# Kernel tuning notes

Hardware: AMD Instinct MI355X
Metric: run time of the kernel (lower is better)

## Reference

```python
import jax, jax.numpy as jnp
import numpy as np

D_MODEL = 1024
N_HEADS = 16
D_HEAD = D_MODEL // N_HEADS
B, T = 2, 2048


def setup_inputs() -> dict:
    key = jax.random.key(0)
    ks = jax.random.split(key, 8)
    s = 1.0 / np.sqrt(D_MODEL)
    return {
        "x": jax.random.normal(ks[0], (B, T, D_MODEL), dtype=jnp.float32),
        "ln_g": jnp.ones((D_MODEL,), jnp.float32),
        "ln_b": jnp.zeros((D_MODEL,), jnp.float32),
        "w_qkv": jax.random.normal(ks[1], (D_MODEL, 3 * D_MODEL), jnp.float32) * s,
        "b_qkv": jnp.zeros((3 * D_MODEL,), jnp.float32),
        "w_gate": jax.random.normal(ks[2], (D_MODEL, D_MODEL), jnp.float32) * s,
        "b_gate": jnp.zeros((D_MODEL,), jnp.float32),
        "w_proj": jax.random.normal(ks[3], (D_MODEL, D_MODEL), jnp.float32) * s,
        "b_proj": jnp.zeros((D_MODEL,), jnp.float32),
    }


def reference(x, ln_g, ln_b, w_qkv, b_qkv, w_gate, b_gate, w_proj, b_proj):
    Bb, Tt, Dd = x.shape
    H, dh = N_HEADS, D_HEAD

    # LayerNorm (eps=1e-5, torch default)
    mu = jnp.mean(x, axis=-1, keepdims=True)
    var = jnp.mean((x - mu) ** 2, axis=-1, keepdims=True)
    x_norm = (x - mu) / jnp.sqrt(var + 1e-5) * ln_g + ln_b

    qkv = x_norm @ w_qkv + b_qkv
    q, k, v = jnp.split(qkv, 3, axis=-1)

    # concept gate on the RAW input x (not x_norm), normalized by its mean
    gate_sig = jax.nn.sigmoid(x @ w_gate + b_gate)
    gate_norm = gate_sig / (jnp.mean(gate_sig, axis=-1, keepdims=True) + 1e-5)
    q = q * gate_norm
    k = k * gate_norm

    # [B,T,D] -> [B,H,T,dh]
    def to_heads(t):
        return t.reshape(Bb, Tt, H, dh).transpose(0, 2, 1, 3)

    q, k, v = to_heads(q), to_heads(k), to_heads(v)

    q = jax.nn.elu(q) + 1.0
    k = jax.nn.elu(k) + 1.0

    # materialized outer-product cumsum (faithful to source formulation)
    kv = jnp.einsum("bhtd,bhtm->bhtdm", k, v)          # [B,H,T,dh,dh]
    kv_cumsum = jnp.cumsum(kv, axis=2)
    out_num = jnp.einsum("bhtd,bhtdm->bhtm", q, kv_cumsum)
    k_cumsum = jnp.cumsum(k, axis=2)
    out_den = jnp.einsum("bhtd,bhtd->bht", q, k_cumsum)[..., None] + 1e-5
    out = out_num / out_den                              # [B,H,T,dh]

    out = out.transpose(0, 2, 1, 3).reshape(Bb, Tt, Dd)
    return out @ w_proj + b_proj
```

## Files before the change

kernel.cpp:

```cpp
#include <hip/hip_runtime.h>
#include <math.h>

constexpr int D      = 1024;
constexpr int H      = 16;
constexpr int DH     = 64;
constexpr int Bb     = 2;
constexpr int T      = 2048;
constexpr int BT     = Bb * T;
constexpr int CHUNK  = 64;
constexpr int NC     = T / CHUNK;
constexpr int LS     = 72;

typedef __attribute__((ext_vector_type(8))) short bf16x8;
typedef __attribute__((ext_vector_type(4))) float f32x4;

#define GLOAD_LDS16(gp, lp) \
    __builtin_amdgcn_global_load_lds((const __attribute__((address_space(1))) void*)(gp), \
                                     (__attribute__((address_space(3))) void*)(lp), 16, 0, 0)

__device__ __forceinline__ short to_bf16(float f) {
    unsigned u = __float_as_uint(f);
    unsigned r = (u + 0x7fffu + ((u >> 16) & 1u)) >> 16;
    return (short)r;
}
__device__ __forceinline__ float bf2f(short s) {
    return __uint_as_float(((unsigned)(unsigned short)s) << 16);
}

__device__ __forceinline__ float block_sum_256(float v, float* sbuf) {
    #pragma unroll
    for (int off = 32; off > 0; off >>= 1) v += __shfl_down(v, off, 64);
    int lane = threadIdx.x & 63;
    int wid  = threadIdx.x >> 6;
    if (lane == 0) sbuf[wid] = v;
    __syncthreads();
    float r = (threadIdx.x < 4) ? sbuf[threadIdx.x] : 0.0f;
    r += __shfl_down(r, 2, 64);
    r += __shfl_down(r, 1, 64);
    if (threadIdx.x == 0) sbuf[0] = r;
    __syncthreads();
    float outv = sbuf[0];
    __syncthreads();
    return outv;
}

__device__ __forceinline__ float elu1(float x) {
    return x > 0.0f ? x + 1.0f : expf(x);
}

__global__ __launch_bounds__(256) void ln_kernel(const float* __restrict__ x,
                                                 const float* __restrict__ g,
                                                 const float* __restrict__ b,
                                                 short* __restrict__ ynb,
                                                 short* __restrict__ xb) {
    __shared__ float sbuf[4];
    int row = blockIdx.x;
    const float* xr = x + (size_t)row * D;
    int c = threadIdx.x * 4;
    float4 xv = *(const float4*)(xr + c);
    float mu = block_sum_256(xv.x + xv.y + xv.z + xv.w, sbuf) * (1.0f / D);
    float d0 = xv.x - mu, d1 = xv.y - mu, d2 = xv.z - mu, d3 = xv.w - mu;
    float var = block_sum_256(d0*d0 + d1*d1 + d2*d2 + d3*d3, sbuf) * (1.0f / D);
    float rstd = rsqrtf(var + 1e-5f);
    float4 gv = *(const float4*)(g + c);
    float4 bv = *(const float4*)(b + c);
    short4 o, xo;
    o.x = to_bf16(d0 * rstd * gv.x + bv.x);
    o.y = to_bf16(d1 * rstd * gv.y + bv.y);
    o.z = to_bf16(d2 * rstd * gv.z + bv.z);
    o.w = to_bf16(d3 * rstd * gv.w + bv.w);
    xo.x = to_bf16(xv.x); xo.y = to_bf16(xv.y);
    xo.z = to_bf16(xv.z); xo.w = to_bf16(xv.w);
    *(short4*)(ynb + (size_t)row * D + c) = o;
    *(short4*)(xb  + (size_t)row * D + c) = xo;
}

__global__ __launch_bounds__(256) void transpose_all_kernel(const float* __restrict__ wq,
                                                            const float* __restrict__ wg,
                                                            const float* __restrict__ wp,
                                                            short* __restrict__ wTcomb,
                                                            short* __restrict__ wTp) {
    __shared__ short tile[32][33];
    int bid = blockIdx.x;
    const float* W; short* Wt; int N; int t;
    if (bid < 3072)      { W = wq; Wt = wTcomb;                        N = 3072; t = bid; }
    else if (bid < 4096) { W = wg; Wt = wTcomb + (size_t)3072 * 1024;  N = 1024; t = bid - 3072; }
    else                 { W = wp; Wt = wTp;                           N = 1024; t = bid - 4096; }
    int ntiles = N >> 5;
    int nb = (t % ntiles) * 32, kb = (t / ntiles) * 32;
    int tx = threadIdx.x & 31, ty = threadIdx.x >> 5;
    #pragma unroll
    for (int i = 0; i < 4; ++i) {
        int k = kb + ty + i * 8;
        tile[ty + i * 8][tx] = to_bf16(W[(size_t)k * N + nb + tx]);
    }
    __syncthreads();
    #pragma unroll
    for (int i = 0; i < 4; ++i) {
        int n = nb + ty + i * 8;
        Wt[(size_t)n * 1024 + kb + tx] = tile[tx][ty + i * 8];
    }
}

__global__ __launch_bounds__(256) void gemm_fused_qkvgate(const short* __restrict__ xnb,
                                                          const short* __restrict__ xb,
                                                          const short* __restrict__ Wt,
                                                          const float* __restrict__ b_qkv,
                                                          const float* __restrict__ b_gate,
                                                          short* __restrict__ qkvb,
                                                          short* __restrict__ gateb) {
    constexpr int BK = 32, K = 1024;
    __shared__ short Als[128 * BK];
    __shared__ short Bls[128 * BK];

    const int tid  = threadIdx.x;
    const int wave = tid >> 6;
    const int lane = tid & 63;
    const int row0 = blockIdx.y * 128;
    const int col0 = blockIdx.x * 128;
    const bool isg = (col0 >= 3 * D);
    const short* A = isg ? xb : xnb;
    const int wm = (wave & 1) * 64;
    const int wn = (wave >> 1) * 64;

    f32x4 acc[4][4] = {};
    const int srow = lane >> 2;
    const int skk  = (lane & 3) * 8;
    const int fr = lane & 15;
    const int fk = (lane >> 4) * 8;

    for (int k0 = 0; k0 < K; k0 += BK) {
        __syncthreads();
        #pragma unroll
        for (int u = 0; u < 2; ++u) {
            int cchunk = wave * 2 + u;
            int r = cchunk * 16 + srow;
            GLOAD_LDS16(A  + (size_t)(row0 + r) * K + k0 + skk, &Als[cchunk * 512]);
            GLOAD_LDS16(Wt + (size_t)(col0 + r) * K + k0 + skk, &Bls[cchunk * 512]);
        }
        __syncthreads();

        bf16x8 af[4], bfr[4];
        #pragma unroll
        for (int i = 0; i < 4; ++i) {
            af[i]  = *(const bf16x8*)&Als[(wm + i * 16 + fr) * BK + fk];
            bfr[i] = *(const bf16x8*)&Bls[(wn + i * 16 + fr) * BK + fk];
        }
        #pragma unroll
        for (int mi = 0; mi < 4; ++mi)
            #pragma unroll
            for (int ni = 0; ni < 4; ++ni)
                acc[mi][ni] = __builtin_amdgcn_mfma_f32_16x16x32_bf16(af[mi], bfr[ni], acc[mi][ni], 0, 0, 0);
    }

    const int ccol  = lane & 15;
    const int crow4 = (lane >> 4) * 4;
    const float* biasp = isg ? (b_gate - 3 * D) : b_qkv;
    short* dst  = isg ? gateb : qkvb;
    const int stride = isg ? D : 3 * D;
    const int csub   = isg ? 3 * D : 0;
    #pragma unroll
    for (int mi = 0; mi < 4; ++mi) {
        #pragma unroll
        for (int ni = 0; ni < 4; ++ni) {
            int col = col0 + wn + ni * 16 + ccol;
            float bv = biasp[col];
            #pragma unroll
            for (int r = 0; r < 4; ++r) {
                int row = row0 + wm + mi * 16 + crow4 + r;
                dst[(size_t)row * stride + (col - csub)] = to_bf16(acc[mi][ni][r] + bv);
            }
        }
    }
}

__global__ __launch_bounds__(256) void gate_apply_inplace(short* __restrict__ qkvb,
                                                          const short* __restrict__ gateb) {
    __shared__ float sbuf[4];
    int row = blockIdx.x;
    int c = threadIdx.x * 4;
    short4 gl = *(const short4*)(gateb + (size_t)row * D + c);
    float s0 = 1.0f / (1.0f + expf(-bf2f(gl.x)));
    float s1 = 1.0f / (1.0f + expf(-bf2f(gl.y)));
    float s2 = 1.0f / (1.0f + expf(-bf2f(gl.z)));
    float s3 = 1.0f / (1.0f + expf(-bf2f(gl.w)));
    float mean = block_sum_256(s0 + s1 + s2 + s3, sbuf) * (1.0f / D);
    float inv = 1.0f / (mean + 1e-5f);
    float g0 = s0 * inv, g1 = s1 * inv, g2 = s2 * inv, g3 = s3 * inv;

    short* qp = qkvb + (size_t)row * (3 * D) + c;
    short* kp = qp + D;
    short4 qv = *(short4*)qp;
    short4 kv = *(short4*)kp;
    qv.x = to_bf16(elu1(bf2f(qv.x) * g0)); qv.y = to_bf16(elu1(bf2f(qv.y) * g1));
    qv.z = to_bf16(elu1(bf2f(qv.z) * g2)); qv.w = to_bf16(elu1(bf2f(qv.w) * g3));
    kv.x = to_bf16(elu1(bf2f(kv.x) * g0)); kv.y = to_bf16(elu1(bf2f(kv.y) * g1));
    kv.z = to_bf16(elu1(bf2f(kv.z) * g2)); kv.w = to_bf16(elu1(bf2f(kv.w) * g3));
    *(short4*)qp = qv;
    *(short4*)kp = kv;
}

__global__ __launch_bounds__(256) void chunk_state_mfma(const short* __restrict__ qkvb,
                                                        float* __restrict__ SxT,
                                                        float* __restrict__ zbuf) {
    __shared__ short Kt[DH * LS];
    __shared__ short Vt[DH * LS];
    int idx = blockIdx.x;
    int c = idx & (NC - 1), h = (idx >> 5) & (H - 1), b = idx >> 9;
    size_t bt0 = (size_t)b * T + c * CHUNK;
    const short* kbase = qkvb + bt0 * (3 * D) + D + h * DH;
    const short* vbase = qkvb + bt0 * (3 * D) + 2 * D + h * DH;
    int tid = threadIdx.x;

    #pragma unroll
    for (int l = 0; l < 2; ++l) {
        int i  = tid + l * 256;
        int t  = i >> 3;
        int d8 = (i & 7) * 8;
        bf16x8 kv = *(const bf16x8*)(kbase + (size_t)t * (3 * D) + d8);
        bf16x8 vv = *(const bf16x8*)(vbase + (size_t)t * (3 * D) + d8);
        #pragma unroll
        for (int j = 0; j < 8; ++j) {
            Kt[(d8 + j) * LS + t] = kv[j];
            Vt[(d8 + j) * LS + t] = vv[j];
        }
    }
    __syncthreads();

    const int wv = tid >> 6, lane = tid & 63;
    const int fr = lane & 15, quad = lane >> 4;
    const int fk = quad * 8, crow4 = quad * 4, ccol = lane & 15;
    const int mbase = wv * 16;

    bf16x8 af[2];
    af[0] = *(const bf16x8*)&Vt[(mbase + fr) * LS + fk];
    af[1] = *(const bf16x8*)&Vt[(mbase + fr) * LS + 32 + fk];

    f32x4 acc[4] = {};
    #pragma unroll
    for (int n = 0; n < 4; ++n) {
        #pragma unroll
        for (int ck = 0; ck < 2; ++ck) {
            bf16x8 bk = *(const bf16x8*)&Kt[(n * 16 + fr) * LS + ck * 32 + fk];
            acc[n] = __builtin_amdgcn_mfma_f32_16x16x32_bf16(af[ck], bk, acc[n], 0, 0, 0);
        }
    }

    float* Sd = SxT + (size_t)idx * (DH * DH);
    #pragma unroll
    for (int n = 0; n < 4; ++n)
        #pragma unroll
        for (int r = 0; r < 4; ++r)
            Sd[(mbase + crow4 + r) * DH + n * 16 + ccol] = acc[n][r];

    if (tid < DH) {
        float zs = 0.0f;
        for (int t = 0; t < CHUNK; ++t) zs += bf2f(Kt[tid * LS + t]);
        zbuf[(size_t)idx * DH + tid] = zs;
    }
}

__global__ __launch_bounds__(256) void chunk_prefix_kernel(const float* __restrict__ S,
                                                           short* __restrict__ Spb,
                                                           float* __restrict__ z) {
    int bh   = blockIdx.x >> 4;
    int part = blockIdx.x & 15;
    int e    = part * 256 + threadIdx.x;
    const float* Sb = S + (size_t)bh * NC * DH * DH;
    short* Pb = Spb + (size_t)bh * NC * DH * DH;
    float acc = 0.0f;
    for (int c = 0; c < NC; ++c) {
        size_t off = (size_t)c * DH * DH + e;
        float t = Sb[off];
        Pb[off] = to_bf16(acc);
        acc += t;
    }
    if (part == 0 && threadIdx.x < DH) {
        float* zb = z + (size_t)bh * NC * DH;
        float za = 0.0f;
        for (int c = 0; c < NC; ++c) {
            float* p = zb + c * DH + threadIdx.x;
            float t = *p; *p = za; za += t;
        }
    }
}

__global__ __launch_bounds__(256) void chunk_attn_mfma(const short* __restrict__ qkvb,
                                                       const short* __restrict__ Spb,
                                                       const float* __restrict__ zbuf,
                                                       short* __restrict__ attnb) {
    __shared__ short Qs[CHUNK * LS];
    __shared__ short Ks[CHUNK * LS];
    __shared__ short Vt[DH * LS];
    __shared__ short Ss[DH * LS];
    __shared__ short As[CHUNK * LS];
    __shared__ float zpL[DH];
    __shared__ float den[CHUNK];

    int idx = blockIdx.x;
    int c = idx & (NC - 1), h = (idx >> 5) & (H - 1), b = idx >> 9;
    size_t bt0 = (size_t)b * T + c * CHUNK;
    const short* qbase = qkvb + bt0 * (3 * D) + h * DH;
    const short* kbase = qbase + D;
    const short* vbase = qbase + 2 * D;
    const short* spb = Spb + (size_t)idx * (DH * DH);
    int tid = threadIdx.x;

    #pragma unroll
    for (int l = 0; l < 2; ++l) {
        int i  = tid + l * 256;
        int t  = i >> 3;
        int d8 = (i & 7) * 8;
        *(bf16x8*)&Qs[t * LS + d8] = *(const bf16x8*)(qbase + (size_t)t * (3 * D) + d8);
        *(bf16x8*)&Ks[t * LS + d8] = *(const bf16x8*)(kbase + (size_t)t * (3 * D) + d8);
        bf16x8 vv = *(const bf16x8*)(vbase + (size_t)t * (3 * D) + d8);
        #pragma unroll
        for (int j = 0; j < 8; ++j) Vt[(d8 + j) * LS + t] = vv[j];
        *(bf16x8*)&Ss[t * LS + d8] = *(const bf16x8*)(spb + (size_t)i * 8);
    }
    if (tid < DH) zpL[tid] = zbuf[(size_t)idx * DH + tid];
    __syncthreads();

    const int wv = tid >> 6, lane = tid & 63;
    const int fr = lane & 15, quad = lane >> 4;
    const int fk = quad * 8, crow4 = quad * 4, ccol = lane & 15;
    const int tbase = wv * 16;

    bf16x8 aq[2];
    aq[0] = *(const bf16x8*)&Qs[(tbase + fr) * LS + fk];
    aq[1] = *(const bf16x8*)&Qs[(tbase + fr) * LS + 32 + fk];

    f32x4 accs[4] = {};
    #pragma unroll
    for (int n = 0; n < 4; ++n) {
        #pragma unroll
        for (int ck = 0; ck < 2; ++ck) {
            bf16x8 bk = *(const bf16x8*)&Ks[(n * 16 + fr) * LS + ck * 32 + fk];
            accs[n] = __builtin_amdgcn_mfma_f32_16x16x32_bf16(aq[ck], bk, accs[n], 0, 0, 0);
        }
    }

    float part[4] = {0.f, 0.f, 0.f, 0.f};
    #pragma unroll
    for (int n = 0; n < 4; ++n) {
        #pragma unroll
        for (int r = 0; r < 4; ++r) {
            int tt = tbase + crow4 + r;
            int ss = n * 16 + ccol;
            float v = (ss <= tt) ? accs[n][r] : 0.0f;
            part[r] += v;
            As[tt * LS + ss] = to_bf16(v);
        }
    }
    #pragma unroll
    for (int r = 0; r < 4; ++r) {
        part[r] += __shfl_xor(part[r], 1, 64);
        part[r] += __shfl_xor(part[r], 2, 64);
        part[r] += __shfl_xor(part[r], 4, 64);
        part[r] += __shfl_xor(part[r], 8, 64);
    }
    if (fr == 0) {
        #pragma unroll
        for (int r = 0; r < 4; ++r) den[tbase + crow4 + r] = part[r];
    }
    __syncthreads();

    if (tid < CHUNK) {
        float qz = 0.0f;
        #pragma unroll 8
        for (int d = 0; d < DH; ++d) qz += bf2f(Qs[tid * LS + d]) * zpL[d];
        den[tid] += qz + 1e-5f;
    }

    f32x4 acco[4] = {};
    #pragma unroll
    for (int m4 = 0; m4 < 4; ++m4) {
        #pragma unroll
        for (int ck = 0; ck < 2; ++ck) {
            bf16x8 bs = *(const bf16x8*)&Ss[(m4 * 16 + fr) * LS + ck * 32 + fk];
            acco[m4] = __builtin_amdgcn_mfma_f32_16x16x32_bf16(aq[ck], bs, acco[m4], 0, 0, 0);
        }
    }
    bf16x8 aa[2];
    aa[0] = *(const bf16x8*)&As[(tbase + fr) * LS + fk];
    aa[1] = *(const bf16x8*)&As[(tbase + fr) * LS + 32 + fk];
    #pragma unroll
    for (int m4 = 0; m4 < 4; ++m4) {
        #pragma unroll
        for (int ck = 0; ck < 2; ++ck) {
            bf16x8 bv = *(const bf16x8*)&Vt[(m4 * 16 + fr) * LS + ck * 32 + fk];
            acco[m4] = __builtin_amdgcn_mfma_f32_16x16x32_bf16(aa[ck], bv, acco[m4], 0, 0, 0);
        }
    }
    __syncthreads();

    short* obase = attnb + bt0 * D + h * DH;
    #pragma unroll
    for (int r = 0; r < 4; ++r) {
        int tt = tbase + crow4 + r;
        float rv = 1.0f / den[tt];
        #pragma unroll
        for (int m4 = 0; m4 < 4; ++m4)
            obase[(size_t)tt * D + m4 * 16 + ccol] = to_bf16(acco[m4][r] * rv);
    }
}

__global__ __launch_bounds__(256) void gemm_proj64(const short* __restrict__ A,
                                                   const short* __restrict__ Bt,
                                                   const float* __restrict__ bias,
                                                   float* __restrict__ C) {
    constexpr int BK = 32, K = 1024, N = 1024;
    __shared__ short Als[64 * BK];
    __shared__ short Bls[128 * BK];

    const int tid  = threadIdx.x;
    const int wave = tid >> 6;
    const int lane = tid & 63;
    const int row0 = blockIdx.y * 64;
    const int col0 = blockIdx.x * 128;
    const int wn = wave * 32;

    f32x4 acc[4][2] = {};
    const int srow = lane >> 2;
    const int skk  = (lane & 3) * 8;
    const int fr = lane & 15;
    const int fk = (lane >> 4) * 8;

    for (int k0 = 0; k0 < K; k0 += BK) {
        __syncthreads();
        #pragma unroll
        for (int u = 0; u < 3; ++u) {
            int cc = wave * 3 + u;
            if (cc < 4) {
                int r = cc * 16 + srow;
                GLOAD_LDS16(A + (size_t)(row0 + r) * K + k0 + skk, &Als[cc * 512]);
            } else {
                int c2 = cc - 4;
                int r = c2 * 16 + srow;
                GLOAD_LDS16(Bt + (size_t)(col0 + r) * K + k0 + skk, &Bls[c2 * 512]);
            }
        }
        __syncthreads();

        bf16x8 af[4], bfr[2];
        #pragma unroll
        for (int i = 0; i < 4; ++i) af[i] = *(const bf16x8*)&Als[(i * 16 + fr) * BK + fk];
        #pragma unroll
        for (int j = 0; j < 2; ++j) bfr[j] = *(const bf16x8*)&Bls[(wn + j * 16 + fr) * BK + fk];
        #pragma unroll
        for (int mi = 0; mi < 4; ++mi)
            #pragma unroll
            for (int ni = 0; ni < 2; ++ni)
                acc[mi][ni] = __builtin_amdgcn_mfma_f32_16x16x32_bf16(af[mi], bfr[ni], acc[mi][ni], 0, 0, 0);
    }

    const int ccol  = lane & 15;
    const int crow4 = (lane >> 4) * 4;
    #pragma unroll
    for (int mi = 0; mi < 4; ++mi) {
        #pragma unroll
        for (int ni = 0; ni < 2; ++ni) {
            int col = col0 + wn + ni * 16 + ccol;
            float bv = bias[col];
            #pragma unroll
            for (int r = 0; r < 4; ++r) {
                int row = row0 + mi * 16 + crow4 + r;
                C[(size_t)row * N + col] = acc[mi][ni][r] + bv;
            }
        }
    }
}

extern "C" void kernel_launch(void* const* d_in, const int* in_sizes, int n_in,
                              void* d_out, int out_size, void* d_ws, size_t ws_size,
                              hipStream_t stream) {
    const float* x      = (const float*)d_in[0];
    const float* ln_g   = (const float*)d_in[1];
    const float* ln_b   = (const float*)d_in[2];
    const float* w_qkv  = (const float*)d_in[3];
    const float* b_qkv  = (const float*)d_in[4];
    const float* w_gate = (const float*)d_in[5];
    const float* b_gate = (const float*)d_in[6];
    const float* w_proj = (const float*)d_in[7];
    const float* b_proj = (const float*)d_in[8];
    float* out = (float*)d_out;

    short* xnb   = (short*)d_ws;
    short* xb    = xnb + (size_t)BT * D;
    short* wTc   = xb + (size_t)BT * D;
    short* wTp   = wTc + (size_t)4096 * 1024;
    short* qkvb  = wTp + (size_t)D * D;
    short* gateb = qkvb + (size_t)BT * 3 * D;
    short* attnb = gateb + (size_t)BT * D;
    float* zbuf  = (float*)(attnb + (size_t)BT * D);
    float* SxT   = (float*)xnb;
    short* Spb   = wTc;

    ln_kernel<<<BT, 256, 0, stream>>>(x, ln_g, ln_b, xnb, xb);
    transpose_all_kernel<<<5120, 256, 0, stream>>>(w_qkv, w_gate, w_proj, wTc, wTp);
    gemm_fused_qkvgate<<<dim3(32, 32), 256, 0, stream>>>(
        xnb, xb, wTc, b_qkv, b_gate, qkvb, gateb);
    gate_apply_inplace<<<BT, 256, 0, stream>>>(qkvb, gateb);
    chunk_state_mfma<<<Bb * H * NC, 256, 0, stream>>>(qkvb, SxT, zbuf);
    chunk_prefix_kernel<<<Bb * H * 16, 256, 0, stream>>>(SxT, Spb, zbuf);
    chunk_attn_mfma<<<Bb * H * NC, 256, 0, stream>>>(qkvb, Spb, zbuf, attnb);
    gemm_proj64<<<dim3(D / 128, BT / 64), 256, 0, stream>>>(attnb, wTp, b_proj, out);
}
```

Before: 209.9 us.

## Merge LN and transpose kernels, deepen GEMM K tiles, fold chunk prefix into attention

Merges the layernorm and weight-transpose kernels into one launch, and doubles the K tile of both GEMMs to 64 so each loop iteration issues twice as many MFMAs per barrier pair. It also removes the separate chunk-prefix kernel: each attention block now sums the preceding chunk states and z vectors from fp32 global memory itself. This saves two launches and a serial prefix pass. In exchange, later chunks read up to 31 prior states each, which is redundant global traffic that grows with chunk index.

```diff
diff --git a/kernel.cpp b/kernel.cpp
--- a/kernel.cpp
+++ b/kernel.cpp
@@ -48,57 +48,59 @@
     return x > 0.0f ? x + 1.0f : expf(x);
 }
 
-__global__ __launch_bounds__(256) void ln_kernel(const float* __restrict__ x,
-                                                 const float* __restrict__ g,
-                                                 const float* __restrict__ b,
-                                                 short* __restrict__ ynb,
-                                                 short* __restrict__ xb) {
+__global__ __launch_bounds__(256) void pre_kernel(const float* __restrict__ x,
+                                                  const float* __restrict__ g,
+                                                  const float* __restrict__ b,
+                                                  const float* __restrict__ wq,
+                                                  const float* __restrict__ wg,
+                                                  const float* __restrict__ wp,
+                                                  short* __restrict__ ynb,
+                                                  short* __restrict__ xbb,
+                                                  short* __restrict__ wTcomb,
+                                                  short* __restrict__ wTp) {
     __shared__ float sbuf[4];
-    int row = blockIdx.x;
-    const float* xr = x + (size_t)row * D;
-    int c = threadIdx.x * 4;
-    float4 xv = *(const float4*)(xr + c);
-    float mu = block_sum_256(xv.x + xv.y + xv.z + xv.w, sbuf) * (1.0f / D);
-    float d0 = xv.x - mu, d1 = xv.y - mu, d2 = xv.z - mu, d3 = xv.w - mu;
-    float var = block_sum_256(d0*d0 + d1*d1 + d2*d2 + d3*d3, sbuf) * (1.0f / D);
-    float rstd = rsqrtf(var + 1e-5f);
-    float4 gv = *(const float4*)(g + c);
-    float4 bv = *(const float4*)(b + c);
-    short4 o, xo;
-    o.x = to_bf16(d0 * rstd * gv.x + bv.x);
-    o.y = to_bf16(d1 * rstd * gv.y + bv.y);
-    o.z = to_bf16(d2 * rstd * gv.z + bv.z);
-    o.w = to_bf16(d3 * rstd * gv.w + bv.w);
-    xo.x = to_bf16(xv.x); xo.y = to_bf16(xv.y);
-    xo.z = to_bf16(xv.z); xo.w = to_bf16(xv.w);
-    *(short4*)(ynb + (size_t)row * D + c) = o;
-    *(short4*)(xb  + (size_t)row * D + c) = xo;
-}
-
-__global__ __launch_bounds__(256) void transpose_all_kernel(const float* __restrict__ wq,
-                                                            const float* __restrict__ wg,
-                                                            const float* __restrict__ wp,
-                                                            short* __restrict__ wTcomb,
-                                                            short* __restrict__ wTp) {
     __shared__ short tile[32][33];
     int bid = blockIdx.x;
-    const float* W; short* Wt; int N; int t;
-    if (bid < 3072)      { W = wq; Wt = wTcomb;                        N = 3072; t = bid; }
-    else if (bid < 4096) { W = wg; Wt = wTcomb + (size_t)3072 * 1024;  N = 1024; t = bid - 3072; }
-    else                 { W = wp; Wt = wTp;                           N = 1024; t = bid - 4096; }
-    int ntiles = N >> 5;
-    int nb = (t % ntiles) * 32, kb = (t / ntiles) * 32;
-    int tx = threadIdx.x & 31, ty = threadIdx.x >> 5;
-    #pragma unroll
-    for (int i = 0; i < 4; ++i) {
-        int k = kb + ty + i * 8;
-        tile[ty + i * 8][tx] = to_bf16(W[(size_t)k * N + nb + tx]);
-    }
-    __syncthreads();
-    #pragma unroll
-    for (int i = 0; i < 4; ++i) {
-        int n = nb + ty + i * 8;
-        Wt[(size_t)n * 1024 + kb + tx] = tile[tx][ty + i * 8];
+    if (bid < BT) {
+        int row = bid;
+        const float* xr = x + (size_t)row * D;
+        int c = threadIdx.x * 4;
+        float4 xv = *(const float4*)(xr + c);
+        float mu = block_sum_256(xv.x + xv.y + xv.z + xv.w, sbuf) * (1.0f / D);
+        float d0 = xv.x - mu, d1 = xv.y - mu, d2 = xv.z - mu, d3 = xv.w - mu;
+        float var = block_sum_256(d0*d0 + d1*d1 + d2*d2 + d3*d3, sbuf) * (1.0f / D);
+        float rstd = rsqrtf(var + 1e-5f);
+        float4 gv = *(const float4*)(g + c);
+        float4 bv = *(const float4*)(b + c);
+        short4 o, xo;
+        o.x = to_bf16(d0 * rstd * gv.x + bv.x);
+        o.y = to_bf16(d1 * rstd * gv.y + bv.y);
+        o.z = to_bf16(d2 * rstd * gv.z + bv.z);
+        o.w = to_bf16(d3 * rstd * gv.w + bv.w);
+        xo.x = to_bf16(xv.x); xo.y = to_bf16(xv.y);
+        xo.z = to_bf16(xv.z); xo.w = to_bf16(xv.w);
+        *(short4*)(ynb + (size_t)row * D + c) = o;
+        *(short4*)(xbb + (size_t)row * D + c) = xo;
+    } else {
+        int t2 = bid - BT;
+        const float* W; short* Wt; int N; int t;
+        if (t2 < 3072)      { W = wq; Wt = wTcomb;                       N = 3072; t = t2; }
+        else if (t2 < 4096) { W = wg; Wt = wTcomb + (size_t)3072 * 1024; N = 1024; t = t2 - 3072; }
+        else                { W = wp; Wt = wTp;                          N = 1024; t = t2 - 4096; }
+        int ntiles = N >> 5;
+        int nb = (t % ntiles) * 32, kb = (t / ntiles) * 32;
+        int tx = threadIdx.x & 31, ty = threadIdx.x >> 5;
+        #pragma unroll
+        for (int i = 0; i < 4; ++i) {
+            int k = kb + ty + i * 8;
+            tile[ty + i * 8][tx] = to_bf16(W[(size_t)k * N + nb + tx]);
+        }
+        __syncthreads();
+        #pragma unroll
+        for (int i = 0; i < 4; ++i) {
+            int n = nb + ty + i * 8;
+            Wt[(size_t)n * 1024 + kb + tx] = tile[tx][ty + i * 8];
+        }
     }
 }
 
@@ -109,7 +111,7 @@
                                                           const float* __restrict__ b_gate,
                                                           short* __restrict__ qkvb,
                                                           short* __restrict__ gateb) {
-    constexpr int BK = 32, K = 1024;
+    constexpr int BK = 64, K = 1024;
     __shared__ short Als[128 * BK];
     __shared__ short Bls[128 * BK];
 
@@ -124,33 +126,36 @@
     const int wn = (wave >> 1) * 64;
 
     f32x4 acc[4][4] = {};
-    const int srow = lane >> 2;
-    const int skk  = (lane & 3) * 8;
+    const int srow = lane >> 3;
+    const int skk  = (lane & 7) * 8;
     const int fr = lane & 15;
     const int fk = (lane >> 4) * 8;
 
     for (int k0 = 0; k0 < K; k0 += BK) {
         __syncthreads();
         #pragma unroll
-        for (int u = 0; u < 2; ++u) {
-            int cchunk = wave * 2 + u;
-            int r = cchunk * 16 + srow;
+        for (int u = 0; u < 4; ++u) {
+            int cchunk = wave * 4 + u;
+            int r = cchunk * 8 + srow;
             GLOAD_LDS16(A  + (size_t)(row0 + r) * K + k0 + skk, &Als[cchunk * 512]);
             GLOAD_LDS16(Wt + (size_t)(col0 + r) * K + k0 + skk, &Bls[cchunk * 512]);
         }
         __syncthreads();
 
-        bf16x8 af[4], bfr[4];
-        #pragma unroll
-        for (int i = 0; i < 4; ++i) {
-            af[i]  = *(const bf16x8*)&Als[(wm + i * 16 + fr) * BK + fk];
-            bfr[i] = *(const bf16x8*)&Bls[(wn + i * 16 + fr) * BK + fk];
-        }
-        #pragma unroll
-        for (int mi = 0; mi < 4; ++mi)
-            #pragma unroll
-            for (int ni = 0; ni < 4; ++ni)
-                acc[mi][ni] = __builtin_amdgcn_mfma_f32_16x16x32_bf16(af[mi], bfr[ni], acc[mi][ni], 0, 0, 0);
+        #pragma unroll
+        for (int h = 0; h < 2; ++h) {
+            bf16x8 af[4], bfr[4];
+            #pragma unroll
+            for (int i = 0; i < 4; ++i) {
+                af[i]  = *(const bf16x8*)&Als[(wm + i * 16 + fr) * BK + h * 32 + fk];
+                bfr[i] = *(const bf16x8*)&Bls[(wn + i * 16 + fr) * BK + h * 32 + fk];
+            }
+            #pragma unroll
+            for (int mi = 0; mi < 4; ++mi)
+                #pragma unroll
+                for (int ni = 0; ni < 4; ++ni)
+                    acc[mi][ni] = __builtin_amdgcn_mfma_f32_16x16x32_bf16(af[mi], bfr[ni], acc[mi][ni], 0, 0, 0);
+        }
     }
 
     const int ccol  = lane & 15;
@@ -201,8 +206,8 @@
 }
 
 __global__ __launch_bounds__(256) void chunk_state_mfma(const short* __restrict__ qkvb,
-                                                        float* __restrict__ SxT,
-                                                        float* __restrict__ zbuf) {
+                                                        float* __restrict__ Sc,
+                                                        float* __restrict__ zc) {
     __shared__ short Kt[DH * LS];
     __shared__ short Vt[DH * LS];
     int idx = blockIdx.x;
@@ -246,7 +251,7 @@
         }
     }
 
-    float* Sd = SxT + (size_t)idx * (DH * DH);
+    float* Sd = Sc + (size_t)idx * (DH * DH);
     #pragma unroll
     for (int n = 0; n < 4; ++n)
         #pragma unroll
@@ -256,38 +261,13 @@
     if (tid < DH) {
         float zs = 0.0f;
         for (int t = 0; t < CHUNK; ++t) zs += bf2f(Kt[tid * LS + t]);
-        zbuf[(size_t)idx * DH + tid] = zs;
-    }
-}
-
-__global__ __launch_bounds__(256) void chunk_prefix_kernel(const float* __restrict__ S,
-                                                           short* __restrict__ Spb,
-                                                           float* __restrict__ z) {
-    int bh   = blockIdx.x >> 4;
-    int part = blockIdx.x & 15;
-    int e    = part * 256 + threadIdx.x;
-    const float* Sb = S + (size_t)bh * NC * DH * DH;
-    short* Pb = Spb + (size_t)bh * NC * DH * DH;
-    float acc = 0.0f;
-    for (int c = 0; c < NC; ++c) {
-        size_t off = (size_t)c * DH * DH + e;
-        float t = Sb[off];
-        Pb[off] = to_bf16(acc);
-        acc += t;
-    }
-    if (part == 0 && threadIdx.x < DH) {
-        float* zb = z + (size_t)bh * NC * DH;
-        float za = 0.0f;
-        for (int c = 0; c < NC; ++c) {
-            float* p = zb + c * DH + threadIdx.x;
-            float t = *p; *p = za; za += t;
-        }
+        zc[(size_t)idx * DH + tid] = zs;
     }
 }
 
 __global__ __launch_bounds__(256) void chunk_attn_mfma(const short* __restrict__ qkvb,
-                                                       const short* __restrict__ Spb,
-                                                       const float* __restrict__ zbuf,
+                                                       const float* __restrict__ Sc,
+                                                       const float* __restrict__ zc,
                                                        short* __restrict__ attnb) {
     __shared__ short Qs[CHUNK * LS];
     __shared__ short Ks[CHUNK * LS];
@@ -303,7 +283,6 @@
     const short* qbase = qkvb + bt0 * (3 * D) + h * DH;
     const short* kbase = qbase + D;
     const short* vbase = qbase + 2 * D;
-    const short* spb = Spb + (size_t)idx * (DH * DH);
     int tid = threadIdx.x;
 
     #pragma unroll
@@ -316,9 +295,38 @@
         bf16x8 vv = *(const bf16x8*)(vbase + (size_t)t * (3 * D) + d8);
         #pragma unroll
         for (int j = 0; j < 8; ++j) Vt[(d8 + j) * LS + t] = vv[j];
-        *(bf16x8*)&Ss[t * LS + d8] = *(const bf16x8*)(spb + (size_t)i * 8);
-    }
-    if (tid < DH) zpL[tid] = zbuf[(size_t)idx * DH + tid];
+    }
+
+    {
+        float acc16[16] = {};
+        const float* Sbh = Sc + (size_t)(idx - c) * (DH * DH);
+        for (int j = 0; j < c; ++j) {
+            const float* Sj = Sbh + (size_t)j * (DH * DH) + tid * 16;
+            #pragma unroll
+            for (int q4 = 0; q4 < 4; ++q4) {
+                float4 v4 = *(const float4*)(Sj + q4 * 4);
+                acc16[q4 * 4 + 0] += v4.x;
+                acc16[q4 * 4 + 1] += v4.y;
+                acc16[q4 * 4 + 2] += v4.z;
+                acc16[q4 * 4 + 3] += v4.w;
+            }
+        }
+        int m0 = tid >> 2, d0 = (tid & 3) * 16;
+        bf16x8 s0v, s1v;
+        #pragma unroll
+        for (int jj = 0; jj < 8; ++jj) {
+            s0v[jj] = to_bf16(acc16[jj]);
+            s1v[jj] = to_bf16(acc16[8 + jj]);
+        }
+        *(bf16x8*)&Ss[m0 * LS + d0]     = s0v;
+        *(bf16x8*)&Ss[m0 * LS + d0 + 8] = s1v;
+    }
+    if (tid < DH) {
+        float zpv = 0.0f;
+        const float* zbh = zc + (size_t)(idx - c) * DH + tid;
+        for (int j = 0; j < c; ++j) zpv += zbh[(size_t)j * DH];
+        zpL[tid] = zpv;
+    }
     __syncthreads();
 
     const int wv = tid >> 6, lane = tid & 63;
@@ -409,7 +417,7 @@
                                                    const short* __restrict__ Bt,
                                                    const float* __restrict__ bias,
                                                    float* __restrict__ C) {
-    constexpr int BK = 32, K = 1024, N = 1024;
+    constexpr int BK = 64, K = 1024, N = 1024;
     __shared__ short Als[64 * BK];
     __shared__ short Bls[128 * BK];
 
@@ -421,37 +429,42 @@
     const int wn = wave * 32;
 
     f32x4 acc[4][2] = {};
-    const int srow = lane >> 2;
-    const int skk  = (lane & 3) * 8;
+    const int srow = lane >> 3;
+    const int skk  = (lane & 7) * 8;
     const int fr = lane & 15;
     const int fk = (lane >> 4) * 8;
 
     for (int k0 = 0; k0 < K; k0 += BK) {
         __syncthreads();
         #pragma unroll
-        for (int u = 0; u < 3; ++u) {
-            int cc = wave * 3 + u;
-            if (cc < 4) {
-                int r = cc * 16 + srow;
+        for (int u = 0; u < 6; ++u) {
+            int cc = wave * 6 + u;
+            if (cc < 8) {
+                int r = cc * 8 + srow;
                 GLOAD_LDS16(A + (size_t)(row0 + r) * K + k0 + skk, &Als[cc * 512]);
             } else {
-                int c2 = cc - 4;
-                int r = c2 * 16 + srow;
+                int c2 = cc - 8;
+                int r = c2 * 8 + srow;
                 GLOAD_LDS16(Bt + (size_t)(col0 + r) * K + k0 + skk, &Bls[c2 * 512]);
             }
         }
         __syncthreads();
 
-        bf16x8 af[4], bfr[2];
-        #pragma unroll
-        for (int i = 0; i < 4; ++i) af[i] = *(const bf16x8*)&Als[(i * 16 + fr) * BK + fk];
-        #pragma unroll
-        for (int j = 0; j < 2; ++j) bfr[j] = *(const bf16x8*)&Bls[(wn + j * 16 + fr) * BK + fk];
-        #pragma unroll
-        for (int mi = 0; mi < 4; ++mi)
-            #pragma unroll
-            for (int ni = 0; ni < 2; ++ni)
-                acc[mi][ni] = __builtin_amdgcn_mfma_f32_16x16x32_bf16(af[mi], bfr[ni], acc[mi][ni], 0, 0, 0);
+        #pragma unroll
+        for (int h = 0; h < 2; ++h) {
+            bf16x8 af[4], bfr[2];
+            #pragma unroll
+            for (int i = 0; i < 4; ++i)
+                af[i] = *(const bf16x8*)&Als[(i * 16 + fr) * BK + h * 32 + fk];
+            #pragma unroll
+            for (int j = 0; j < 2; ++j)
+                bfr[j] = *(const bf16x8*)&Bls[(wn + j * 16 + fr) * BK + h * 32 + fk];
+            #pragma unroll
+            for (int mi = 0; mi < 4; ++mi)
+                #pragma unroll
+                for (int ni = 0; ni < 2; ++ni)
+                    acc[mi][ni] = __builtin_amdgcn_mfma_f32_16x16x32_bf16(af[mi], bfr[ni], acc[mi][ni], 0, 0, 0);
+        }
     }
 
     const int ccol  = lane & 15;
@@ -492,17 +505,15 @@
     short* qkvb  = wTp + (size_t)D * D;
     short* gateb = qkvb + (size_t)BT * 3 * D;
     short* attnb = gateb + (size_t)BT * D;
-    float* zbuf  = (float*)(attnb + (size_t)BT * D);
-    float* SxT   = (float*)xnb;
-    short* Spb   = wTc;
-
-    ln_kernel<<<BT, 256, 0, stream>>>(x, ln_g, ln_b, xnb, xb);
-    transpose_all_kernel<<<5120, 256, 0, stream>>>(w_qkv, w_gate, w_proj, wTc, wTp);
+    float* zc    = (float*)(attnb + (size_t)BT * D);
+    float* Sc    = (float*)xnb;
+
+    pre_kernel<<<BT + 5120, 256, 0, stream>>>(x, ln_g, ln_b, w_qkv, w_gate, w_proj,
+                                              xnb, xb, wTc, wTp);
     gemm_fused_qkvgate<<<dim3(32, 32), 256, 0, stream>>>(
         xnb, xb, wTc, b_qkv, b_gate, qkvb, gateb);
     gate_apply_inplace<<<BT, 256, 0, stream>>>(qkvb, gateb);
-    chunk_state_mfma<<<Bb * H * NC, 256, 0, stream>>>(qkvb, SxT, zbuf);
-    chunk_prefix_kernel<<<Bb * H * 16, 256, 0, stream>>>(SxT, Spb, zbuf);
-    chunk_attn_mfma<<<Bb * H * NC, 256, 0, stream>>>(qkvb, Spb, zbuf, attnb);
+    chunk_state_mfma<<<Bb * H * NC, 256, 0, stream>>>(qkvb, Sc, zc);
+    chunk_attn_mfma<<<Bb * H * NC, 256, 0, stream>>>(qkvb, Sc, zc, attnb);
     gemm_proj64<<<dim3(D / 128, BT / 64), 256, 0, stream>>>(attnb, wTp, b_proj, out);
 }
```

Result: slower. 248.1 us (+18.2%).
